# Performance work log

Hardware: AMD Instinct MI355X
Metric: run time of the kernel (lower is better)

## Reference

```python
import jax, jax.numpy as jnp
import numpy as np

B, N, DEG = 4, 2048, 16
HID, NH = 768, 12
D = HID // NH
N_REL = 64
E = B * N * DEG


def setup_inputs() -> dict:
    key = jax.random.key(0)
    k_x, k_r, k_q, k_k, k_v, k_e = jax.random.split(key, 6)
    node_states = jax.random.normal(k_x, (B, N, HID), dtype=jnp.float32) * 0.02
    # Deterministically unique edges: each (b, i) attends to DEG distinct tails.
    b_idx = jnp.repeat(jnp.arange(B), N * DEG)
    i_idx = jnp.tile(jnp.repeat(jnp.arange(N), DEG), B)
    offs = jnp.tile(jnp.arange(1, DEG + 1), B * N)
    t_idx = (i_idx + offs) % N
    r_idx = jax.random.randint(k_r, (E,), 0, N_REL)
    edge_indices = jnp.stack([b_idx, i_idx, t_idx, r_idx]).astype(jnp.int32)
    # Linear params (torch: y = x @ W.T + b)
    Wq = jax.random.normal(k_q, (HID, HID), dtype=jnp.float32) * 0.02
    Wk = jax.random.normal(k_k, (HID, HID), dtype=jnp.float32) * 0.02
    Wv = jax.random.normal(k_v, (HID, HID), dtype=jnp.float32) * 0.02
    bq = jnp.zeros((HID,), jnp.float32)
    bk = jnp.zeros((HID,), jnp.float32)
    bv = jnp.zeros((HID,), jnp.float32)
    rel_emb = jax.random.normal(k_e, (N_REL, HID), dtype=jnp.float32) * 0.02
    rel_emb = rel_emb.at[0].set(0.0)  # TOKEN_TO_TOKEN_RELATION_ID zeroed
    return {"node_states": node_states, "edge_indices": edge_indices,
            "Wq": Wq, "bq": bq, "Wk": Wk, "bk": bk, "Wv": Wv, "bv": bv,
            "rel_emb": rel_emb}


def reference(node_states, edge_indices, Wq, bq, Wk, bk, Wv, bv, rel_emb):
    Bv, Nv, H = node_states.shape
    Q = node_states @ Wq.T + bq
    K = node_states @ Wk.T + bk
    V = node_states @ Wv.T + bv
    b, i, t, r = edge_indices[0], edge_indices[1], edge_indices[2], edge_indices[3]
    # Translated key: K[b, tail] - relation embedding
    k_shift = (K[b, t] - rel_emb[r]).reshape(-1, NH, D)  # (E, nh, d)
    q_e = Q[b, i].reshape(-1, NH, D)                      # (E, nh, d)
    scale = jnp.sqrt(jnp.asarray(D, node_states.dtype))
    logits = jnp.einsum('ehd,ehd->eh', q_e, k_shift) / scale  # (E, nh)
    # Sparse softmax over tail dim == segment softmax per (batch, head node)
    seg = b * Nv + i
    n_seg = Bv * Nv
    m = jax.ops.segment_max(logits, seg, num_segments=n_seg)
    ex = jnp.exp(logits - m[seg])
    den = jax.ops.segment_sum(ex, seg, num_segments=n_seg)
    probs = ex / den[seg]  # (E, nh); dropout is identity in eval
    # Aggregate: out[b, i] += probs * V[b, t]
    Vt = V.reshape(Bv, Nv, NH, D)
    contrib = probs[:, :, None] * Vt[b, t]  # (E, nh, d)
    out = jax.ops.segment_sum(contrib, seg, num_segments=n_seg)
    return out.reshape(Bv, Nv, H)
```

## Files before the change

### kernel.cpp

```cpp
#include <hip/hip_runtime.h>

#define B_    4
#define N_    2048
#define HID_  768
#define NH_   12
#define E_    131072
#define M_    8192
#define NREL_ 64
#define G_    16
#define BAND_ 32
#define VP_   40
#define PP_   40

typedef unsigned short u16;
typedef unsigned int   u32;
typedef short bf16x8 __attribute__((ext_vector_type(8)));
typedef float f32x4  __attribute__((ext_vector_type(4)));

__device__ __forceinline__ u16 f2bf(float x) {
  u32 u = __float_as_uint(x);
  u += 0x7fffu + ((u >> 16) & 1u);
  return (u16)(u >> 16);
}
__device__ __forceinline__ float bflo(u32 u) { return __uint_as_float(u << 16); }
__device__ __forceinline__ float bfhi(u32 u) { return __uint_as_float(u & 0xffff0000u); }
__device__ __forceinline__ float bf1(u16 v) { return __uint_as_float(((u32)v) << 16); }

__device__ __forceinline__ void load_lds16(const u16* g, u16* l) {
  __builtin_amdgcn_global_load_lds((__attribute__((address_space(1))) void*)(g),
                                   (__attribute__((address_space(3))) void*)(l),
                                   16, 0, 0);
}

__global__ __launch_bounds__(256) void k_convert(
    const float4* __restrict__ X, const float4* __restrict__ Wq,
    const float4* __restrict__ Wk, const float4* __restrict__ Wv,
    const float4* __restrict__ rel,
    ushort4* __restrict__ Xbf, ushort4* __restrict__ Wbf, ushort4* __restrict__ Rbf) {
  const int NX4 = (M_ * HID_) / 4;
  const int NW4 = (HID_ * HID_) / 4;
  const int NR4 = (NREL_ * HID_) / 4;
  int tid = blockIdx.x * 256 + threadIdx.x;
  const float4* src; ushort4* dst; int off;
  if (tid < NX4) { src = X; dst = Xbf; off = tid; }
  else if (tid < NX4 + 3 * NW4) {
    int t2 = tid - NX4;
    int wi = t2 / NW4;
    off = t2 - wi * NW4;
    src = (wi == 0) ? Wq : (wi == 1) ? Wk : Wv;
    dst = Wbf + (size_t)wi * NW4;
  } else {
    off = tid - NX4 - 3 * NW4;
    if (off >= NR4) return;
    src = rel; dst = Rbf;
  }
  float4 v = src[off];
  ushort4 o;
  o.x = f2bf(v.x); o.y = f2bf(v.y); o.z = f2bf(v.z); o.w = f2bf(v.w);
  dst[off] = o;
}

__global__ __launch_bounds__(512, 2) void k_gemm(
    const u16* __restrict__ Xbf, const u16* __restrict__ Wbf,
    const float* __restrict__ bq, const float* __restrict__ bk, const float* __restrict__ bv,
    u16* __restrict__ Qb, u16* __restrict__ Kb, u16* __restrict__ Vb) {
  extern __shared__ __align__(16) u16 lds[];
  const int tid = threadIdx.x;
  const int w = tid >> 6, lane = tid & 63;
  const int lm = lane & 15, lg = lane >> 4;
  const int wm = w >> 1, wn = w & 1;
  const int m0  = blockIdx.x * 256;
  const int n0g = blockIdx.y * 288;

  f32x4 acc[4][9] = {};

  auto STAGE = [&](int bi, int kt) {
    const int k0 = kt * 32;
    u16* Ab = lds + bi * (256 * 32);
    u16* Bb = lds + 3 * (256 * 32) + bi * (288 * 32);
#pragma unroll
    for (int ii = 0; ii < 2; ++ii) {
      const int sb = (ii * 8 + w) * 64;
      const int s  = sb + lane;
      const int m  = s >> 2;
      const int g  = (s & 3) ^ ((m >> 1) & 3);
      load_lds16(Xbf + (size_t)(m0 + m) * HID_ + k0 + g * 8, Ab + sb * 8);
    }
#pragma unroll
    for (int ii = 0; ii < 2; ++ii) {
      const int sb = (ii * 8 + w) * 64;
      const int s  = sb + lane;
      const int m  = s >> 2;
      const int g  = (s & 3) ^ ((m >> 1) & 3);
      load_lds16(Wbf + (size_t)(n0g + m) * HID_ + k0 + g * 8, Bb + sb * 8);
    }
    if (w < 2) {
      const int sb = (16 + w) * 64;
      const int s  = sb + lane;
      const int m  = s >> 2;
      const int g  = (s & 3) ^ ((m >> 1) & 3);
      load_lds16(Wbf + (size_t)(n0g + m) * HID_ + k0 + g * 8, Bb + sb * 8);
    }
  };

  auto COMPUTE = [&](int bi) {
    const u16* As = lds + bi * (256 * 32);
    const u16* Bs = lds + 3 * (256 * 32) + bi * (288 * 32);
    bf16x8 bfv[9];
#pragma unroll
    for (int nt = 0; nt < 9; ++nt) {
      const int n = wn * 144 + nt * 16 + lm;
      const int g = lg ^ ((n >> 1) & 3);
      bfv[nt] = *(const bf16x8*)&Bs[n * 32 + g * 8];
    }
    __builtin_amdgcn_s_setprio(1);
#pragma unroll
    for (int mt = 0; mt < 4; ++mt) {
      const int m = wm * 64 + mt * 16 + lm;
      const int g = lg ^ ((m >> 1) & 3);
      bf16x8 af = *(const bf16x8*)&As[m * 32 + g * 8];
#pragma unroll
      for (int nt = 0; nt < 9; ++nt)
        acc[mt][nt] = __builtin_amdgcn_mfma_f32_16x16x32_bf16(af, bfv[nt], acc[mt][nt], 0, 0, 0);
    }
    __builtin_amdgcn_s_setprio(0);
  };

#define BODYK(KT, BC, BS, DOSTAGE, VMZ)                                  \
  do {                                                                   \
    if (VMZ)        asm volatile("s_waitcnt vmcnt(0)" ::: "memory");     \
    else if (w < 2) asm volatile("s_waitcnt vmcnt(5)" ::: "memory");     \
    else            asm volatile("s_waitcnt vmcnt(4)" ::: "memory");     \
    __builtin_amdgcn_s_barrier();                                        \
    asm volatile("" ::: "memory");                                       \
    if (DOSTAGE) STAGE(BS, (KT) + 2);                                    \
    COMPUTE(BC);                                                         \
  } while (0)

  STAGE(0, 0);
  STAGE(1, 1);
  for (int t3 = 0; t3 < 21; t3 += 3) {
    BODYK(t3 + 0, 0, 2, true, false);
    BODYK(t3 + 1, 1, 0, true, false);
    BODYK(t3 + 2, 2, 1, true, false);
  }
  BODYK(21, 0, 2, true,  false);
  BODYK(22, 1, 0, false, false);
  BODYK(23, 2, 1, false, true);
#undef BODYK

#pragma unroll
  for (int nt = 0; nt < 9; ++nt) {
    const int c    = n0g + wn * 144 + nt * 16 + lm;
    const int widx = (c >= 1536) ? 2 : (c >= 768) ? 1 : 0;
    const int col  = c - widx * 768;
    const float bb = ((widx == 0) ? bq : (widx == 1) ? bk : bv)[col];
    u16* Op = (widx == 0) ? Qb : (widx == 1) ? Kb : Vb;
#pragma unroll
    for (int mt = 0; mt < 4; ++mt) {
      const int rbase = m0 + wm * 64 + mt * 16 + lg * 4;
#pragma unroll
      for (int r = 0; r < 4; ++r)
        Op[(size_t)(rbase + r) * HID_ + col] = f2bf(acc[mt][nt][r] + bb);
    }
  }
}

__global__ __launch_bounds__(256) void k_qrel(
    const u16* __restrict__ Qb, const u16* __restrict__ Rbf, u16* __restrict__ QRelb) {
  const int tid = threadIdx.x, w = tid >> 6, lane = tid & 63;
  const int lm = lane & 15, quad = lane >> 4;
  const int m0 = blockIdx.x * 32 + (w & 1) * 16;
  const int h0 = (w >> 1) * 6;
#pragma unroll
  for (int hh = 0; hh < 6; ++hh) {
    const int h = h0 + hh;
    const u16* qp = Qb + (size_t)(m0 + lm) * HID_ + h * 64 + quad * 8;
    bf16x8 a0 = *(const bf16x8*)(qp);
    bf16x8 a1 = *(const bf16x8*)(qp + 32);
#pragma unroll
    for (int rt = 0; rt < 4; ++rt) {
      const u16* rp = Rbf + (size_t)(rt * 16 + lm) * HID_ + h * 64 + quad * 8;
      bf16x8 b0 = *(const bf16x8*)(rp);
      bf16x8 b1 = *(const bf16x8*)(rp + 32);
      f32x4 c = {0.f, 0.f, 0.f, 0.f};
      c = __builtin_amdgcn_mfma_f32_16x16x32_bf16(a0, b0, c, 0, 0, 0);
      c = __builtin_amdgcn_mfma_f32_16x16x32_bf16(a1, b1, c, 0, 0, 0);
#pragma unroll
      for (int r = 0; r < 4; ++r)
        QRelb[(size_t)(m0 + quad * 4 + r) * HID_ + h * 64 + rt * 16 + lm] = f2bf(c[r]);
    }
  }
}

__global__ __launch_bounds__(256, 2) void k_attn(
    const u16* __restrict__ Qb, const u16* __restrict__ Kb, const u16* __restrict__ Vb,
    const u16* __restrict__ QRelb, const int* __restrict__ eidx,
    float* __restrict__ out) {
  __shared__ __align__(16) u16 Vt[HID_ * VP_];
  __shared__ __align__(16) u16 p_bf[NH_ * 16 * PP_];
  __shared__ u16 r_s[256];
  __shared__ int t_s[256];
  __shared__ int badf;

  const int tid = threadIdx.x;
  const int w = tid >> 6, lane = tid & 63;
  const int lm = lane & 15, quad = lane >> 4;
  const int e0b = blockIdx.x * 256;
  const int b  = eidx[e0b];
  const int i0 = eidx[E_ + e0b];
  const int bN = b * N_;

  const int sV = tid & 31, pV = tid >> 5;
  const int rowV = (i0 + 1 + sV) & (N_ - 1);
  const u16* srcV = Vb + (size_t)(bN + rowV) * HID_ + pV * 96;
  uint4 vv[12];
#pragma unroll
  for (int c = 0; c < 12; ++c) vv[c] = *(const uint4*)(srcV + c * 8);

  const u16* Qrow  = Qb + (size_t)(bN + i0 + lm) * HID_ + quad * 8;
  const u16* Krow0 = Kb + (size_t)(bN + ((i0 + 1 + lm) & (N_ - 1))) * HID_ + quad * 8;
  const u16* Krow1 = Kb + (size_t)(bN + ((i0 + 17 + lm) & (N_ - 1))) * HID_ + quad * 8;
  bf16x8 qa[3][2], ka[3][4];
#pragma unroll
  for (int hh = 0; hh < 3; ++hh) {
    const int o = (w * 3 + hh) * 64;
    qa[hh][0] = *(const bf16x8*)(Qrow + o);
    qa[hh][1] = *(const bf16x8*)(Qrow + o + 32);
    ka[hh][0] = *(const bf16x8*)(Krow0 + o);
    ka[hh][1] = *(const bf16x8*)(Krow0 + o + 32);
    ka[hh][2] = *(const bf16x8*)(Krow1 + o);
    ka[hh][3] = *(const bf16x8*)(Krow1 + o + 32);
  }

  const int t_own = eidx[2 * E_ + e0b + tid];
  const int r_own = eidx[3 * E_ + e0b + tid];
  t_s[tid] = t_own;
  r_s[tid] = (u16)r_own;
  if (tid == 0) badf = 0;
  {
    u32* pz = (u32*)p_bf;
#pragma unroll
    for (int z = 0; z < NH_ * 16 * PP_ / 2 / 256; ++z) pz[z * 256 + tid] = 0;
    const int expect = (i0 + (tid >> 4) + (tid & 15) + 1) & (N_ - 1);
    if (t_own != expect) badf = 1;
  }
  __syncthreads();
  const int bad = badf;

  if (!bad) {
#pragma unroll
    for (int c = 0; c < 12; ++c) {
      uint4 v = vv[c];
      const int d0 = pV * 96 + c * 8;
      Vt[(d0 + 0) * VP_ + sV] = (u16)(v.x);
      Vt[(d0 + 1) * VP_ + sV] = (u16)(v.x >> 16);
      Vt[(d0 + 2) * VP_ + sV] = (u16)(v.y);
      Vt[(d0 + 3) * VP_ + sV] = (u16)(v.y >> 16);
      Vt[(d0 + 4) * VP_ + sV] = (u16)(v.z);
      Vt[(d0 + 5) * VP_ + sV] = (u16)(v.z >> 16);
      Vt[(d0 + 6) * VP_ + sV] = (u16)(v.w);
      Vt[(d0 + 7) * VP_ + sV] = (u16)(v.w >> 16);
    }

    int eidx4[4]; float qrelv[3][4];
#pragma unroll
    for (int r = 0; r < 4; ++r) {
      const int il = quad * 4 + r;
      eidx4[r] = il * 16 + ((lm - il) & 15);
    }
#pragma unroll
    for (int hh = 0; hh < 3; ++hh) {
      const int h = w * 3 + hh;
#pragma unroll
      for (int r = 0; r < 4; ++r) {
        const int il = quad * 4 + r;
        qrelv[hh][r] = bf1(QRelb[(size_t)(bN + i0 + il) * HID_ + h * 64 + r_s[eidx4[r]]]);
      }
    }

#pragma unroll
    for (int hh = 0; hh < 3; ++hh) {
      const int h = w * 3 + hh;
      f32x4 c0 = {0.f, 0.f, 0.f, 0.f}, c1 = {0.f, 0.f, 0.f, 0.f};
      c0 = __builtin_amdgcn_mfma_f32_16x16x32_bf16(qa[hh][0], ka[hh][0], c0, 0, 0, 0);
      c0 = __builtin_amdgcn_mfma_f32_16x16x32_bf16(qa[hh][1], ka[hh][1], c0, 0, 0, 0);
      c1 = __builtin_amdgcn_mfma_f32_16x16x32_bf16(qa[hh][0], ka[hh][2], c1, 0, 0, 0);
      c1 = __builtin_amdgcn_mfma_f32_16x16x32_bf16(qa[hh][1], ka[hh][3], c1, 0, 0, 0);
#pragma unroll
      for (int r = 0; r < 4; ++r) {
        const int il = quad * 4 + r;
        const float val = (lm >= il) ? c0[r] : c1[r];
        const float ex = __expf((val - qrelv[hh][r]) * 0.125f);
        float den = ex;
        den += __shfl_xor(den, 1);
        den += __shfl_xor(den, 2);
        den += __shfl_xor(den, 4);
        den += __shfl_xor(den, 8);
        const float p = ex * __builtin_amdgcn_rcpf(den);
        const int slot = il + ((lm - il) & 15);
        p_bf[(h * 16 + il) * PP_ + slot] = f2bf(p);
      }
    }
    __syncthreads();

#pragma unroll
    for (int hh = 0; hh < 3; ++hh) {
      const int h = w * 3 + hh;
      bf16x8 af = *(const bf16x8*)&p_bf[(h * 16 + lm) * PP_ + quad * 8];
#pragma unroll
      for (int nt = 0; nt < 4; ++nt) {
        bf16x8 bv = *(const bf16x8*)&Vt[(h * 64 + nt * 16 + lm) * VP_ + quad * 8];
        f32x4 d = {0.f, 0.f, 0.f, 0.f};
        d = __builtin_amdgcn_mfma_f32_16x16x32_bf16(af, bv, d, 0, 0, 0);
#pragma unroll
        for (int r = 0; r < 4; ++r)
          out[(size_t)(bN + i0 + quad * 4 + r) * HID_ + h * 64 + nt * 16 + lm] = d[r];
      }
    }
  } else {
    const int il = tid >> 4;
#pragma unroll
    for (int h = 0; h < NH_; ++h) {
      const u16* qp = Qb + (size_t)(bN + i0 + il) * HID_ + h * 64;
      const u16* kp = Kb + (size_t)(bN + t_own) * HID_ + h * 64;
      float s = 0.f;
      for (int d = 0; d < 64; ++d) s += bf1(qp[d]) * bf1(kp[d]);
      const float qrel = bf1(QRelb[(size_t)(bN + i0 + il) * HID_ + h * 64 + r_own]);
      const float ex = __expf((s - qrel) * 0.125f);
      float den = ex;
      den += __shfl_xor(den, 1);
      den += __shfl_xor(den, 2);
      den += __shfl_xor(den, 4);
      den += __shfl_xor(den, 8);
      p_bf[tid * NH_ + h] = f2bf(ex * __builtin_amdgcn_rcpf(den));
    }
    __syncthreads();
#pragma unroll
    for (int gsub = 0; gsub < 4; ++gsub) {
      const int il2 = w * 4 + gsub;
      float a0[8] = {0.f,0.f,0.f,0.f,0.f,0.f,0.f,0.f};
      float a1[8] = {0.f,0.f,0.f,0.f,0.f,0.f,0.f,0.f};
      for (int j2 = 0; j2 < 16; ++j2) {
        const int t2 = t_s[il2 * 16 + j2];
        const u16* Vrow = Vb + (size_t)(bN + t2) * HID_;
        uint4 v0 = *(const uint4*)(Vrow + lane * 8);
        const float p0 = bf1(p_bf[(il2 * 16 + j2) * NH_ + (lane >> 3)]);
        a0[0] += p0 * bflo(v0.x); a0[1] += p0 * bfhi(v0.x);
        a0[2] += p0 * bflo(v0.y); a0[3] += p0 * bfhi(v0.y);
        a0[4] += p0 * bflo(v0.z); a0[5] += p0 * bfhi(v0.z);
        a0[6] += p0 * bflo(v0.w); a0[7] += p0 * bfhi(v0.w);
        if (lane < 32) {
          uint4 v1 = *(const uint4*)(Vrow + 512 + lane * 8);
          const float p1 = bf1(p_bf[(il2 * 16 + j2) * NH_ + 8 + (lane >> 3)]);
          a1[0] += p1 * bflo(v1.x); a1[1] += p1 * bfhi(v1.x);
          a1[2] += p1 * bflo(v1.y); a1[3] += p1 * bfhi(v1.y);
          a1[4] += p1 * bflo(v1.z); a1[5] += p1 * bfhi(v1.z);
          a1[6] += p1 * bflo(v1.w); a1[7] += p1 * bfhi(v1.w);
        }
      }
      float* orow = out + (size_t)(bN + i0 + il2) * HID_;
      *(float4*)(orow + lane * 8)     = make_float4(a0[0], a0[1], a0[2], a0[3]);
      *(float4*)(orow + lane * 8 + 4) = make_float4(a0[4], a0[5], a0[6], a0[7]);
      if (lane < 32) {
        *(float4*)(orow + 512 + lane * 8)     = make_float4(a1[0], a1[1], a1[2], a1[3]);
        *(float4*)(orow + 512 + lane * 8 + 4) = make_float4(a1[4], a1[5], a1[6], a1[7]);
      }
    }
  }
}

extern "C" void kernel_launch(void* const* d_in, const int* in_sizes, int n_in,
                              void* d_out, int out_size, void* d_ws, size_t ws_size,
                              hipStream_t stream) {
  const float* X   = (const float*)d_in[0];
  const int*   eidx= (const int*)d_in[1];
  const float* Wq  = (const float*)d_in[2];
  const float* bq  = (const float*)d_in[3];
  const float* Wk  = (const float*)d_in[4];
  const float* bk  = (const float*)d_in[5];
  const float* Wv  = (const float*)d_in[6];
  const float* bv  = (const float*)d_in[7];
  const float* rel = (const float*)d_in[8];
  float* out = (float*)d_out;

  char* ws = (char*)d_ws;
  u16* Xbf = (u16*)(ws);
  u16* QRelb = Xbf;
  u16* Wbf = (u16*)(ws + 12582912);
  u16* Qb  = (u16*)(ws + 16121856);
  u16* Kb  = (u16*)(ws + 28704768);
  u16* Vb  = (u16*)(ws + 41287680);
  u16* Rbf = (u16*)(ws + 53870592);

  static bool s_attr = false;
  if (!s_attr) {
    (void)hipFuncSetAttribute((const void*)k_gemm,
                              hipFuncAttributeMaxDynamicSharedMemorySize, 104448);
    s_attr = true;
  }

  k_convert<<<7920, 256, 0, stream>>>((const float4*)X, (const float4*)Wq,
                                      (const float4*)Wk, (const float4*)Wv,
                                      (const float4*)rel,
                                      (ushort4*)Xbf, (ushort4*)Wbf, (ushort4*)Rbf);
  k_gemm<<<dim3(32, 8), 512, 104448, stream>>>(Xbf, Wbf, bq, bk, bv, Qb, Kb, Vb);
  k_qrel<<<256, 256, 0, stream>>>(Qb, Rbf, QRelb);
  k_attn<<<512, 256, 0, stream>>>(Qb, Kb, Vb, QRelb, eidx, out);
}
```

Baseline: 153.8 us.

## Split GEMM K-tile into three interleaved load/MFMA phases with ping-pong barriers

```diff
diff --git a/kernel.cpp b/kernel.cpp
--- a/kernel.cpp
+++ b/kernel.cpp
@@ -74,80 +74,110 @@
 
   f32x4 acc[4][9] = {};
 
-  auto STAGE = [&](int bi, int kt) {
-    const int k0 = kt * 32;
-    u16* Ab = lds + bi * (256 * 32);
-    u16* Bb = lds + 3 * (256 * 32) + bi * (288 * 32);
-#pragma unroll
-    for (int ii = 0; ii < 2; ++ii) {
-      const int sb = (ii * 8 + w) * 64;
-      const int s  = sb + lane;
-      const int m  = s >> 2;
-      const int g  = (s & 3) ^ ((m >> 1) & 3);
-      load_lds16(Xbf + (size_t)(m0 + m) * HID_ + k0 + g * 8, Ab + sb * 8);
-    }
-#pragma unroll
-    for (int ii = 0; ii < 2; ++ii) {
-      const int sb = (ii * 8 + w) * 64;
-      const int s  = sb + lane;
-      const int m  = s >> 2;
-      const int g  = (s & 3) ^ ((m >> 1) & 3);
-      load_lds16(Wbf + (size_t)(n0g + m) * HID_ + k0 + g * 8, Bb + sb * 8);
-    }
-    if (w < 2) {
-      const int sb = (16 + w) * 64;
-      const int s  = sb + lane;
-      const int m  = s >> 2;
-      const int g  = (s & 3) ^ ((m >> 1) & 3);
-      load_lds16(Wbf + (size_t)(n0g + m) * HID_ + k0 + g * 8, Bb + sb * 8);
-    }
-  };
-
-  auto COMPUTE = [&](int bi) {
-    const u16* As = lds + bi * (256 * 32);
-    const u16* Bs = lds + 3 * (256 * 32) + bi * (288 * 32);
-    bf16x8 bfv[9];
-#pragma unroll
-    for (int nt = 0; nt < 9; ++nt) {
-      const int n = wn * 144 + nt * 16 + lm;
-      const int g = lg ^ ((n >> 1) & 3);
-      bfv[nt] = *(const bf16x8*)&Bs[n * 32 + g * 8];
-    }
-    __builtin_amdgcn_s_setprio(1);
-#pragma unroll
-    for (int mt = 0; mt < 4; ++mt) {
-      const int m = wm * 64 + mt * 16 + lm;
-      const int g = lg ^ ((m >> 1) & 3);
-      bf16x8 af = *(const bf16x8*)&As[m * 32 + g * 8];
-#pragma unroll
-      for (int nt = 0; nt < 9; ++nt)
-        acc[mt][nt] = __builtin_amdgcn_mfma_f32_16x16x32_bf16(af, bfv[nt], acc[mt][nt], 0, 0, 0);
-    }
-    __builtin_amdgcn_s_setprio(0);
-  };
-
-#define BODYK(KT, BC, BS, DOSTAGE, VMZ)                                  \
-  do {                                                                   \
-    if (VMZ)        asm volatile("s_waitcnt vmcnt(0)" ::: "memory");     \
-    else if (w < 2) asm volatile("s_waitcnt vmcnt(5)" ::: "memory");     \
-    else            asm volatile("s_waitcnt vmcnt(4)" ::: "memory");     \
-    __builtin_amdgcn_s_barrier();                                        \
-    asm volatile("" ::: "memory");                                       \
-    if (DOSTAGE) STAGE(BS, (KT) + 2);                                    \
-    COMPUTE(BC);                                                         \
+#define STAGE_A(BI, KT) do {                                              \
+    const int k0_ = (KT) * 32;                                            \
+    u16* Ab_ = lds + (BI) * (256 * 32);                                   \
+    _Pragma("unroll")                                                     \
+    for (int ii = 0; ii < 2; ++ii) {                                      \
+      const int sb_ = (ii * 8 + w) * 64;                                  \
+      const int s_  = sb_ + lane;                                         \
+      const int m_  = s_ >> 2;                                            \
+      const int g_  = (s_ & 3) ^ ((m_ >> 1) & 3);                         \
+      load_lds16(Xbf + (size_t)(m0 + m_) * HID_ + k0_ + g_ * 8, Ab_ + sb_ * 8); \
+    }                                                                     \
   } while (0)
 
-  STAGE(0, 0);
-  STAGE(1, 1);
+#define STAGE_B(BI, KT) do {                                              \
+    const int k0_ = (KT) * 32;                                            \
+    u16* Bb_ = lds + 3 * (256 * 32) + (BI) * (288 * 32);                  \
+    _Pragma("unroll")                                                     \
+    for (int ii = 0; ii < 2; ++ii) {                                      \
+      const int sb_ = (ii * 8 + w) * 64;                                  \
+      const int s_  = sb_ + lane;                                         \
+      const int m_  = s_ >> 2;                                            \
+      const int g_  = (s_ & 3) ^ ((m_ >> 1) & 3);                         \
+      load_lds16(Wbf + (size_t)(n0g + m_) * HID_ + k0_ + g_ * 8, Bb_ + sb_ * 8); \
+    }                                                                     \
+  } while (0)
+
+#define STAGE_BT(BI, KT) do {                                             \
+    if (w < 2) {                                                          \
+      const int k0_ = (KT) * 32;                                          \
+      u16* Bb_ = lds + 3 * (256 * 32) + (BI) * (288 * 32);                \
+      const int sb_ = (16 + w) * 64;                                      \
+      const int s_  = sb_ + lane;                                         \
+      const int m_  = s_ >> 2;                                            \
+      const int g_  = (s_ & 3) ^ ((m_ >> 1) & 3);                         \
+      load_lds16(Wbf + (size_t)(n0g + m_) * HID_ + k0_ + g_ * 8, Bb_ + sb_ * 8); \
+    }                                                                     \
+  } while (0)
+
+#define PHASE(AS, BSP, AF, NT0, FIRST, STGSTMT, WAITSTMT) do {            \
+    bf16x8 bfv_[3];                                                       \
+    if (FIRST) {                                                          \
+      _Pragma("unroll")                                                   \
+      for (int mt = 0; mt < 4; ++mt) {                                    \
+        const int m_ = wm * 64 + mt * 16 + lm;                            \
+        const int g_ = lg ^ ((m_ >> 1) & 3);                              \
+        AF[mt] = *(const bf16x8*)&(AS)[m_ * 32 + g_ * 8];                 \
+      }                                                                   \
+    }                                                                     \
+    _Pragma("unroll")                                                     \
+    for (int k = 0; k < 3; ++k) {                                         \
+      const int n_ = wn * 144 + ((NT0) + k) * 16 + lm;                    \
+      const int g_ = lg ^ ((n_ >> 1) & 3);                                \
+      bfv_[k] = *(const bf16x8*)&(BSP)[n_ * 32 + g_ * 8];                 \
+    }                                                                     \
+    STGSTMT;                                                              \
+    WAITSTMT;                                                             \
+    __builtin_amdgcn_s_barrier();                                         \
+    asm volatile("s_waitcnt lgkmcnt(0)" ::: "memory");                    \
+    __builtin_amdgcn_sched_barrier(0);                                    \
+    __builtin_amdgcn_s_setprio(1);                                        \
+    _Pragma("unroll")                                                     \
+    for (int mt = 0; mt < 4; ++mt)                                        \
+      _Pragma("unroll")                                                   \
+      for (int k = 0; k < 3; ++k)                                         \
+        acc[mt][(NT0) + k] = __builtin_amdgcn_mfma_f32_16x16x32_bf16(AF[mt], bfv_[k], acc[mt][(NT0) + k], 0, 0, 0); \
+    __builtin_amdgcn_s_setprio(0);                                        \
+    __builtin_amdgcn_s_barrier();                                         \
+  } while (0)
+
+#define TILE(T, BC, BSS, DOSTG, WMODE) do {                               \
+    const u16* As_ = lds + (BC) * (256 * 32);                             \
+    const u16* Bs_ = lds + 3 * (256 * 32) + (BC) * (288 * 32);            \
+    bf16x8 af_[4];                                                        \
+    PHASE(As_, Bs_, af_, 0, true,  { if (DOSTG) STAGE_A(BSS, (T) + 2); }, {}); \
+    PHASE(As_, Bs_, af_, 3, false, { if (DOSTG) STAGE_B(BSS, (T) + 2); }, {}); \
+    PHASE(As_, Bs_, af_, 6, false, { if (DOSTG) STAGE_BT(BSS, (T) + 2); },     \
+          { if ((WMODE) == 0) {                                           \
+              if (w < 2) asm volatile("s_waitcnt vmcnt(5)" ::: "memory"); \
+              else       asm volatile("s_waitcnt vmcnt(4)" ::: "memory"); \
+            } else if ((WMODE) == 1) {                                    \
+              asm volatile("s_waitcnt vmcnt(0)" ::: "memory");            \
+            } });                                                         \
+  } while (0)
+
+  STAGE_A(0, 0); STAGE_B(0, 0); STAGE_BT(0, 0);
+  STAGE_A(1, 1); STAGE_B(1, 1); STAGE_BT(1, 1);
+  if (w < 2) asm volatile("s_waitcnt vmcnt(5)" ::: "memory");
+  else       asm volatile("s_waitcnt vmcnt(4)" ::: "memory");
+  __builtin_amdgcn_s_barrier();
+
   for (int t3 = 0; t3 < 21; t3 += 3) {
-    BODYK(t3 + 0, 0, 2, true, false);
-    BODYK(t3 + 1, 1, 0, true, false);
-    BODYK(t3 + 2, 2, 1, true, false);
-  }
-  BODYK(21, 0, 2, true,  false);
-  BODYK(22, 1, 0, false, false);
-  BODYK(23, 2, 1, false, true);
-#undef BODYK
+    TILE(t3 + 0, 0, 2, true, 0);
+    TILE(t3 + 1, 1, 0, true, 0);
+    TILE(t3 + 2, 2, 1, true, 0);
+  }
+  TILE(21, 0, 2, true,  0);
+  TILE(22, 1, 0, false, 1);
+  TILE(23, 2, 1, false, 2);
+
+#undef TILE
+#undef PHASE
+#undef STAGE_BT
+#undef STAGE_B
+#undef STAGE_A
 
 #pragma unroll
   for (int nt = 0; nt < 9; ++nt) {
```

Result: slower. 158.5 us (+3.1%).
